# Kernel tuning notes

Hardware: AMD Instinct MI355X
Metric: run time of the kernel (lower is better)

Reference implementation:

```python
import jax, jax.numpy as jnp
import numpy as np

B, S, D, H = 2, 2048, 1024, 16
D_H = D // H  # 64


def setup_inputs() -> dict:
    key = jax.random.key(0)
    ks = jax.random.split(key, 12)
    inp = {
        "query": jax.random.normal(ks[0], (B, S, D), dtype=jnp.float32),
        "key":   jax.random.normal(ks[1], (B, S, D), dtype=jnp.float32),
        "value": jax.random.normal(ks[2], (B, S, D), dtype=jnp.float32),
        # causal 0/1 float mask, broadcastable to [B, H, Sq, Sk]; 1 = masked
        "mask":  jnp.broadcast_to(jnp.triu(jnp.ones((S, S), dtype=jnp.float32), k=1)[None, None], (B, 1, S, S)),
    }
    scale = 0.02
    inp["wq"] = jax.random.normal(ks[3], (D, D), dtype=jnp.float32) * scale
    inp["bq"] = jnp.zeros((D,), dtype=jnp.float32)
    inp["wk"] = jax.random.normal(ks[4], (D, D), dtype=jnp.float32) * scale
    inp["bk"] = jnp.zeros((D,), dtype=jnp.float32)
    inp["wv"] = jax.random.normal(ks[5], (D, D), dtype=jnp.float32) * scale
    inp["bv"] = jnp.zeros((D,), dtype=jnp.float32)
    inp["wff"] = jax.random.normal(ks[6], (D, D), dtype=jnp.float32) * scale
    inp["bff"] = jnp.zeros((D,), dtype=jnp.float32)
    return inp


def _split_head(x):
    # [B, S, D] -> [B, H, S, d_h]
    b, s, _ = x.shape
    return x.reshape(b, s, H, D_H).transpose(0, 2, 1, 3)


def reference(query, key, value, mask, wq, bq, wk, bk, wv, bv, wff, bff):
    # QKV projections (torch Linear: x @ W.T + b)
    q = _split_head(query @ wq.T + bq)
    k = _split_head(key @ wk.T + bk)
    v = _split_head(value @ wv.T + bv)
    # scaled dot-product attention
    scores = jnp.einsum("bhqd,bhkd->bhqk", q, k) / jnp.sqrt(jnp.float32(D_H))
    scores = scores + mask * (-1e9)
    attn = jax.nn.softmax(scores, axis=-1)
    out = jnp.einsum("bhqk,bhkd->bhqd", attn, v)
    # concat heads: [B, H, S, d_h] -> [B, S, D]
    out = out.transpose(0, 2, 1, 3).reshape(query.shape[0], query.shape[1], D)
    return out @ wff.T + bff
```

## Files before the change

kernel.cpp:

```cpp
#include <hip/hip_runtime.h>
#include <hip/hip_bf16.h>

#define B_  2
#define S_  2048
#define D_  1024
#define H_  16
#define DH_ 64
#define M_  (B_ * S_)

using bf16x8 = __attribute__((ext_vector_type(8))) short;
using s16x4  = __attribute__((ext_vector_type(4))) short;
using f32x4  = __attribute__((ext_vector_type(4))) float;

__device__ __forceinline__ bf16x8 ldg8(const __hip_bfloat16* p) {
    bf16x8 v;
    __builtin_memcpy(&v, p, 16);
    return v;
}
__device__ __forceinline__ bf16x8 lds8(const __hip_bfloat16* p) {
    bf16x8 v;
    __builtin_memcpy(&v, p, 16);
    return v;
}
__device__ __forceinline__ void gll16(const void* g, void* l) {
    __builtin_amdgcn_global_load_lds(
        (const __attribute__((address_space(1))) unsigned int*)g,
        (__attribute__((address_space(3))) unsigned int*)l,
        16, 0, 0);
}
__device__ __forceinline__ short bf16bits(float x) {
    __hip_bfloat16 hv = __float2bfloat16(x);
    short sv;
    __builtin_memcpy(&sv, &hv, 2);
    return sv;
}
__device__ __forceinline__ unsigned cvtpk(float lo, float hi) {
    unsigned r;
    asm("v_cvt_pk_bf16_f32 %0, %1, %2" : "=v"(r) : "v"(lo), "v"(hi));
    return r;
}

__global__ void cvt_all(const float* __restrict__ q, const float* __restrict__ k,
                        const float* __restrict__ v, const float* __restrict__ wq,
                        const float* __restrict__ wk, const float* __restrict__ wv,
                        const float* __restrict__ wff,
                        __hip_bfloat16* __restrict__ Xq, __hip_bfloat16* __restrict__ Xk,
                        __hip_bfloat16* __restrict__ Xv, __hip_bfloat16* __restrict__ Wq,
                        __hip_bfloat16* __restrict__ Wk, __hip_bfloat16* __restrict__ Wv,
                        __hip_bfloat16* __restrict__ Wf) {
    const size_t e = (size_t)(blockIdx.x * 256 + threadIdx.x) * 8;
    const float* src;
    __hip_bfloat16* dst;
    size_t off;
    if (e < ((size_t)3 << 22)) {
        const int i = (int)(e >> 22);
        off = e & (((size_t)1 << 22) - 1);
        src = (i == 0) ? q : (i == 1) ? k : v;
        dst = (i == 0) ? Xq : (i == 1) ? Xk : Xv;
    } else {
        const size_t e2 = e - ((size_t)3 << 22);
        const int i = (int)(e2 >> 20);
        off = e2 & (((size_t)1 << 20) - 1);
        src = (i == 0) ? wq : (i == 1) ? wk : (i == 2) ? wv : wff;
        dst = (i == 0) ? Wq : (i == 1) ? Wk : (i == 2) ? Wv : Wf;
    }
    float4 a, b;
    __builtin_memcpy(&a, src + off, 16);
    __builtin_memcpy(&b, src + off + 4, 16);
    __hip_bfloat16 h[8];
    h[0] = __float2bfloat16(a.x); h[1] = __float2bfloat16(a.y);
    h[2] = __float2bfloat16(a.z); h[3] = __float2bfloat16(a.w);
    h[4] = __float2bfloat16(b.x); h[5] = __float2bfloat16(b.y);
    h[6] = __float2bfloat16(b.z); h[7] = __float2bfloat16(b.w);
    __builtin_memcpy(dst + off, h, 16);
}

template<int MI>
__device__ __forceinline__
void gemm_body(const __hip_bfloat16* __restrict__ A,
               const __hip_bfloat16* __restrict__ W,
               const float* __restrict__ bias,
               void* __restrict__ out, int mode, float oscale,
               int row0, int col0) {
    constexpr int K  = D_;
    constexpr int N  = D_;
    constexpr int TM = MI * 32;
    __shared__ __hip_bfloat16 At[2][TM][32];
    __shared__ __hip_bfloat16 Wt[2][128][32];

    const int tid = threadIdx.x;
    const int w   = tid >> 6;
    const int l   = tid & 63;
    const int lr  = l & 15;
    const int lg  = l >> 4;
    const int wr  = (w >> 1) * (MI * 16);
    const int wc  = (w & 1) * 64;

    const int srow   = l >> 2;
    const int schunk = l & 3;

    f32x4 acc[MI][4] = {};

    auto STAGE = [&](int buf, int k0) {
#pragma unroll
        for (int r = 0; r < TM / 64; ++r) {
            const int row = r * 64 + w * 16 + srow;
            const int csw = (schunk ^ (row & 3)) * 8;
            gll16(A + (size_t)(row0 + row) * K + k0 + csw, &At[buf][r * 64 + w * 16][0]);
        }
#pragma unroll
        for (int r = 0; r < 2; ++r) {
            const int row = r * 64 + w * 16 + srow;
            const int csw = (schunk ^ (row & 3)) * 8;
            gll16(W + (size_t)(col0 + row) * K + k0 + csw, &Wt[buf][r * 64 + w * 16][0]);
        }
    };

    STAGE(0, 0);
    int cur = 0;
    for (int k0 = 0; k0 < K; k0 += 32) {
        __syncthreads();
        if (k0 + 32 < K) STAGE(cur ^ 1, k0 + 32);
        bf16x8 af[MI], wf[4];
#pragma unroll
        for (int m = 0; m < MI; ++m) {
            const int arow = wr + m * 16 + lr;
            af[m] = lds8(&At[cur][arow][(lg ^ (arow & 3)) * 8]);
        }
#pragma unroll
        for (int n = 0; n < 4; ++n) {
            const int wrow = wc + n * 16 + lr;
            wf[n] = lds8(&Wt[cur][wrow][(lg ^ (wrow & 3)) * 8]);
        }
#pragma unroll
        for (int m = 0; m < MI; ++m)
#pragma unroll
            for (int n = 0; n < 4; ++n)
                acc[m][n] = __builtin_amdgcn_mfma_f32_16x16x32_bf16(
                    af[m], wf[n], acc[m][n], 0, 0, 0);
        cur ^= 1;
    }

    float bv[4];
#pragma unroll
    for (int n = 0; n < 4; ++n) bv[n] = bias[col0 + wc + n * 16 + lr];

    if (mode == 1) {
#pragma unroll
        for (int m = 0; m < MI; ++m) {
            const int row_s = row0 + wr + m * 16 + lg * 4;
            const int bq = row_s >> 11, s0 = row_s & (S_ - 1);
#pragma unroll
            for (int n = 0; n < 4; ++n) {
                const int col = col0 + wc + n * 16 + lr;
                const int h = col >> 6, d = col & (DH_ - 1);
                s16x4 pk;
#pragma unroll
                for (int r = 0; r < 4; ++r) pk[r] = bf16bits(acc[m][n][r] + bv[n]);
                __builtin_memcpy(
                    (__hip_bfloat16*)out + ((size_t)((bq * H_ + h) * DH_) + d) * S_ + s0,
                    &pk, 8);
            }
        }
    } else {
#pragma unroll
        for (int m = 0; m < MI; ++m)
#pragma unroll
            for (int n = 0; n < 4; ++n)
#pragma unroll
                for (int r = 0; r < 4; ++r) {
                    const int row = row0 + wr + m * 16 + lg * 4 + r;
                    const int col = col0 + wc + n * 16 + lr;
                    const float v = acc[m][n][r] + bv[n];
                    if (mode == 0)
                        ((__hip_bfloat16*)out)[(size_t)row * N + col] =
                            __float2bfloat16(v * oscale);
                    else
                        ((float*)out)[(size_t)row * N + col] = v;
                }
    }
}

__global__ __launch_bounds__(256)
void gemm_qkv(const __hip_bfloat16* __restrict__ Xq, const __hip_bfloat16* __restrict__ Xk,
              const __hip_bfloat16* __restrict__ Xv, const __hip_bfloat16* __restrict__ Wq,
              const __hip_bfloat16* __restrict__ Wk, const __hip_bfloat16* __restrict__ Wv,
              const float* __restrict__ bq, const float* __restrict__ bk,
              const float* __restrict__ bv,
              __hip_bfloat16* __restrict__ Qp, __hip_bfloat16* __restrict__ Kp,
              __hip_bfloat16* __restrict__ Vt) {
    const int z = blockIdx.z;
    const __hip_bfloat16* A = (z == 0) ? Xq : (z == 1) ? Xk : Xv;
    const __hip_bfloat16* W = (z == 0) ? Wq : (z == 1) ? Wk : Wv;
    const float* bias       = (z == 0) ? bq : (z == 1) ? bk : bv;
    void* out               = (z == 0) ? (void*)Qp : (z == 1) ? (void*)Kp : (void*)Vt;
    const float osc = (z == 0) ? 0.125f * 1.4426950408889634f : 1.f;

    const int lin  = blockIdx.y * 8 + blockIdx.x;
    const int xcd  = lin & 7;
    const int idx  = lin >> 3;
    const int row0 = (xcd * 4 + (idx & 3)) * 128;
    const int col0 = (idx >> 2) * 128;

    gemm_body<4>(A, W, bias, out, (z == 2) ? 1 : 0, osc, row0, col0);
}

__global__ __launch_bounds__(256)
void gemm_ff(const __hip_bfloat16* __restrict__ A, const __hip_bfloat16* __restrict__ W,
             const float* __restrict__ bias, float* __restrict__ out) {
    const int lin  = blockIdx.y * 8 + blockIdx.x;
    const int xcd  = lin & 7;
    const int idx  = lin >> 3;
    const int row0 = (xcd * 8 + (idx & 7)) * 64;
    const int col0 = (idx >> 3) * 128;
    gemm_body<2>(A, W, bias, out, 2, 1.f, row0, col0);
}

__global__ __launch_bounds__(512)
void attn_fwd(const __hip_bfloat16* __restrict__ Qp,
              const __hip_bfloat16* __restrict__ Kp,
              const __hip_bfloat16* __restrict__ Vt,
              __hip_bfloat16* __restrict__ O) {
    __shared__ __hip_bfloat16 Kt[2][64][64];
    __shared__ __hip_bfloat16 Vs[2][64][64];
    __shared__ __hip_bfloat16 Pl[8][16][64];

    const int tid = threadIdx.x;
    const int w   = tid >> 6;
    const int l   = tid & 63;
    const int lr  = l & 15;
    const int lg  = l >> 4;

    const int raw = blockIdx.x;
    const int wg  = (raw & 7) * 64 + (raw >> 3);
    const int xcd = wg >> 6;
    const int loc = wg & 63;
    const int bhi = loc >> 4;
    const int prr = loc & 15;
    const int pr  = (bhi >= 2) ? (15 - prr) : prr;
    const int bh  = xcd * 4 + bhi;
    const int h   = bh & (H_ - 1);
    const int b   = bh >> 4;

    const int sub  = w >> 2;
    const int qb_s = sub ? (31 - pr) : pr;
    const int qw0  = qb_s * 64 + (w & 3) * 16;

    bf16x8 aq[2];
#pragma unroll
    for (int kc = 0; kc < 2; ++kc)
        aq[kc] = ldg8(Qp + (size_t)(b * S_ + qw0 + lr) * D_ + h * DH_ + kc * 32 + lg * 8);

    f32x4 o[4] = {};
    f32x4 rs4 = {};

    const int nkt_max = 32 - pr;

    const int srow   = l >> 3;
    const int schunk = l & 7;
    const int psw    = (lr & 7) << 4;

    auto STAGE = [&](int buf, int kt) {
        const int k0 = kt * 64;
        const int row = w * 8 + srow;
        const int csw = (schunk ^ (row & 7)) * 8;
        gll16(Kp + (size_t)(b * S_ + k0 + row) * D_ + h * DH_ + csw,
              &Kt[buf][w * 8][0]);
        gll16(Vt + ((size_t)((b * H_ + h) * DH_) + row) * S_ + k0 + csw,
              &Vs[buf][w * 8][0]);
    };

    char* prow = (char*)&Pl[w][lr][0];

    auto STEP = [&](int kt, int cur) {
        const int k0 = kt * 64;
        __syncthreads();
        if (kt + 1 < nkt_max) STAGE(cur ^ 1, kt + 1);

        if (kt <= qb_s) {
            f32x4 sc[4] = {};
            __builtin_amdgcn_s_setprio(1);
#pragma unroll
            for (int kk = 0; kk < 4; ++kk) {
                const int krow = kk * 16 + lr;
#pragma unroll
                for (int kc = 0; kc < 2; ++kc) {
                    bf16x8 kf = lds8(&Kt[cur][krow][((kc * 4 + lg) ^ (krow & 7)) * 8]);
                    sc[kk] = __builtin_amdgcn_mfma_f32_16x16x32_bf16(kf, aq[kc], sc[kk], 0, 0, 0);
                }
            }
            __builtin_amdgcn_s_setprio(0);

            const int qrow = qw0 + lr;
            if (kt == qb_s) {
#pragma unroll
                for (int kk = 0; kk < 4; ++kk) {
                    float pv[4];
#pragma unroll
                    for (int r = 0; r < 4; ++r) {
                        const int key = k0 + kk * 16 + lg * 4 + r;
                        pv[r] = (key > qrow) ? 0.f : exp2f(sc[kk][r]);
                        rs4[r] += pv[r];
                    }
                    unsigned uu[2] = { cvtpk(pv[0], pv[1]), cvtpk(pv[2], pv[3]) };
                    __builtin_memcpy(prow + ((kk * 32 + lg * 8) ^ psw), uu, 8);
                }
            } else {
#pragma unroll
                for (int kk = 0; kk < 4; ++kk) {
                    float pv[4];
#pragma unroll
                    for (int r = 0; r < 4; ++r) {
                        pv[r] = exp2f(sc[kk][r]);
                        rs4[r] += pv[r];
                    }
                    unsigned uu[2] = { cvtpk(pv[0], pv[1]), cvtpk(pv[2], pv[3]) };
                    __builtin_memcpy(prow + ((kk * 32 + lg * 8) ^ psw), uu, 8);
                }
            }

            bf16x8 pa[2];
#pragma unroll
            for (int kc = 0; kc < 2; ++kc)
                __builtin_memcpy(&pa[kc], prow + ((kc * 64 + lg * 16) ^ psw), 16);
            __builtin_amdgcn_s_setprio(1);
#pragma unroll
            for (int j = 0; j < 4; ++j) {
                const int vrow = j * 16 + lr;
#pragma unroll
                for (int kc = 0; kc < 2; ++kc) {
                    bf16x8 vf = lds8(&Vs[cur][vrow][((kc * 4 + lg) ^ (vrow & 7)) * 8]);
                    o[j] = __builtin_amdgcn_mfma_f32_16x16x32_bf16(pa[kc], vf, o[j], 0, 0, 0);
                }
            }
            __builtin_amdgcn_s_setprio(0);
        }
    };

    STAGE(0, 0);
    for (int kt = 0; kt < nkt_max; kt += 2) {
        STEP(kt, 0);
        if (kt + 1 < nkt_max) STEP(kt + 1, 1);
    }

    float rsf = rs4[0] + rs4[1] + rs4[2] + rs4[3];
    rsf += __shfl_xor(rsf, 16);
    rsf += __shfl_xor(rsf, 32);
#pragma unroll
    for (int r = 0; r < 4; ++r) {
        const float inv = 1.f / __shfl(rsf, 4 * lg + r);
        const int row = qw0 + 4 * lg + r;
#pragma unroll
        for (int j = 0; j < 4; ++j)
            O[((size_t)(b * S_ + row)) * D_ + h * DH_ + j * 16 + lr] =
                __float2bfloat16(o[j][r] * inv);
    }
}

extern "C" void kernel_launch(void* const* d_in, const int* in_sizes, int n_in,
                              void* d_out, int out_size, void* d_ws, size_t ws_size,
                              hipStream_t stream) {
    const float* q    = (const float*)d_in[0];
    const float* kin  = (const float*)d_in[1];
    const float* vin  = (const float*)d_in[2];
    const float* wq   = (const float*)d_in[4];
    const float* bq   = (const float*)d_in[5];
    const float* wk   = (const float*)d_in[6];
    const float* bk   = (const float*)d_in[7];
    const float* wv   = (const float*)d_in[8];
    const float* bv   = (const float*)d_in[9];
    const float* wff  = (const float*)d_in[10];
    const float* bff  = (const float*)d_in[11];

    char* ws = (char*)d_ws;
    const size_t MB = 1024 * 1024;
    __hip_bfloat16* Xq  = (__hip_bfloat16*)(ws + 0 * MB);
    __hip_bfloat16* Xk  = (__hip_bfloat16*)(ws + 8 * MB);
    __hip_bfloat16* Xv  = (__hip_bfloat16*)(ws + 16 * MB);
    __hip_bfloat16* Wqb = (__hip_bfloat16*)(ws + 24 * MB);
    __hip_bfloat16* Wkb = (__hip_bfloat16*)(ws + 26 * MB);
    __hip_bfloat16* Wvb = (__hip_bfloat16*)(ws + 28 * MB);
    __hip_bfloat16* Wfb = (__hip_bfloat16*)(ws + 30 * MB);
    __hip_bfloat16* Qp  = (__hip_bfloat16*)(ws + 32 * MB);
    __hip_bfloat16* Kp  = (__hip_bfloat16*)(ws + 40 * MB);
    __hip_bfloat16* Vt  = (__hip_bfloat16*)(ws + 48 * MB);
    __hip_bfloat16* Ob  = (__hip_bfloat16*)(ws + 56 * MB);

    cvt_all<<<8192, 256, 0, stream>>>(q, kin, vin, wq, wk, wv, wff,
                                      Xq, Xk, Xv, Wqb, Wkb, Wvb, Wfb);

    dim3 gq(8, 32, 3);
    gemm_qkv<<<gq, 256, 0, stream>>>(Xq, Xk, Xv, Wqb, Wkb, Wvb,
                                     bq, bk, bv, Qp, Kp, Vt);

    attn_fwd<<<512, 512, 0, stream>>>(Qp, Kp, Vt, Ob);

    dim3 gg(8, 64);
    gemm_ff<<<gg, 256, 0, stream>>>(Ob, Wfb, bff, (float*)d_out);
}
```

Baseline: 119.6 us.

## Balance causal attention work by splitting high query block keys across wave groups

Each workgroup still owns a paired low and high query block, but the work is now split differently. The first four waves process the low block and then the first part of the high block's key range. The second four waves process the remaining key tiles of the high block, and each group has its own double-buffered K/V stream. At the end the partial outputs and row sums are combined through shared memory, which replaces the earlier pattern where half the waves sat idle on masked tiles. In exchange the kernel uses twice the LDS for K/V, adds a cross-group reduction, and relies on softmax without a running max, since the partial sums are added directly.

```diff
diff --git a/kernel.cpp b/kernel.cpp
--- a/kernel.cpp
+++ b/kernel.cpp
@@ -221,8 +221,8 @@
               const __hip_bfloat16* __restrict__ Kp,
               const __hip_bfloat16* __restrict__ Vt,
               __hip_bfloat16* __restrict__ O) {
-    __shared__ __hip_bfloat16 Kt[2][64][64];
-    __shared__ __hip_bfloat16 Vs[2][64][64];
+    __shared__ __hip_bfloat16 Kt[2][2][64][64];
+    __shared__ __hip_bfloat16 Vs[2][2][64][64];
     __shared__ __hip_bfloat16 Pl[8][16][64];
 
     const int tid = threadIdx.x;
@@ -230,130 +230,182 @@
     const int l   = tid & 63;
     const int lr  = l & 15;
     const int lg  = l >> 4;
+    const int grp = w >> 2;
+    const int wi  = w & 3;
 
     const int raw = blockIdx.x;
     const int wg  = (raw & 7) * 64 + (raw >> 3);
-    const int xcd = wg >> 6;
-    const int loc = wg & 63;
-    const int bhi = loc >> 4;
-    const int prr = loc & 15;
-    const int pr  = (bhi >= 2) ? (15 - prr) : prr;
-    const int bh  = xcd * 4 + bhi;
+    const int bh  = wg >> 4;
+    const int pr  = wg & 15;
     const int h   = bh & (H_ - 1);
     const int b   = bh >> 4;
 
-    const int sub  = w >> 2;
-    const int qb_s = sub ? (31 - pr) : pr;
-    const int qw0  = qb_s * 64 + (w & 3) * 16;
-
-    bf16x8 aq[2];
-#pragma unroll
-    for (int kc = 0; kc < 2; ++kc)
-        aq[kc] = ldg8(Qp + (size_t)(b * S_ + qw0 + lr) * D_ + h * DH_ + kc * 32 + lg * 8);
-
-    f32x4 o[4] = {};
-    f32x4 rs4 = {};
-
-    const int nkt_max = 32 - pr;
+    const int qbL = pr, qbH = 31 - pr;
+    const int qwL = qbL * 64 + wi * 16;
+    const int qwH = qbH * 64 + wi * 16;
 
     const int srow   = l >> 3;
     const int schunk = l & 7;
     const int psw    = (lr & 7) << 4;
 
-    auto STAGE = [&](int buf, int kt) {
+    bf16x8 aqH[2], aqL[2];
+#pragma unroll
+    for (int kc = 0; kc < 2; ++kc)
+        aqH[kc] = ldg8(Qp + (size_t)(b * S_ + qwH + lr) * D_ + h * DH_ + kc * 32 + lg * 8);
+    if (grp == 0) {
+#pragma unroll
+        for (int kc = 0; kc < 2; ++kc)
+            aqL[kc] = ldg8(Qp + (size_t)(b * S_ + qwL + lr) * D_ + h * DH_ + kc * 32 + lg * 8);
+    }
+
+    f32x4 oH[4] = {}, oL[4] = {};
+    f32x4 rsH4 = {}, rsL4 = {};
+
+    auto STAGE = [&](int stream, int buf, int kt) {
         const int k0 = kt * 64;
-        const int row = w * 8 + srow;
-        const int csw = (schunk ^ (row & 7)) * 8;
-        gll16(Kp + (size_t)(b * S_ + k0 + row) * D_ + h * DH_ + csw,
-              &Kt[buf][w * 8][0]);
-        gll16(Vt + ((size_t)((b * H_ + h) * DH_) + row) * S_ + k0 + csw,
-              &Vs[buf][w * 8][0]);
+#pragma unroll
+        for (int r = 0; r < 2; ++r) {
+            const int row = wi * 16 + r * 8 + srow;
+            const int csw = (schunk ^ (row & 7)) * 8;
+            gll16(Kp + (size_t)(b * S_ + k0 + row) * D_ + h * DH_ + csw,
+                  &Kt[stream][buf][wi * 16 + r * 8][0]);
+            gll16(Vt + ((size_t)((b * H_ + h) * DH_) + row) * S_ + k0 + csw,
+                  &Vs[stream][buf][wi * 16 + r * 8][0]);
+        }
     };
 
     char* prow = (char*)&Pl[w][lr][0];
 
-    auto STEP = [&](int kt, int cur) {
+    auto UNIT = [&](int stream, int curb, int kt, const bf16x8 (&aq)[2],
+                    f32x4 (&o)[4], f32x4& rs4, int qw0, bool diag) {
         const int k0 = kt * 64;
+        f32x4 sc[4] = {};
+        __builtin_amdgcn_s_setprio(1);
+#pragma unroll
+        for (int kk = 0; kk < 4; ++kk) {
+            const int krow = kk * 16 + lr;
+#pragma unroll
+            for (int kc = 0; kc < 2; ++kc) {
+                bf16x8 kf = lds8(&Kt[stream][curb][krow][((kc * 4 + lg) ^ (krow & 7)) * 8]);
+                sc[kk] = __builtin_amdgcn_mfma_f32_16x16x32_bf16(kf, aq[kc], sc[kk], 0, 0, 0);
+            }
+        }
+        __builtin_amdgcn_s_setprio(0);
+
+        const int qrow = qw0 + lr;
+        if (diag) {
+#pragma unroll
+            for (int kk = 0; kk < 4; ++kk) {
+                float pv[4];
+#pragma unroll
+                for (int r = 0; r < 4; ++r) {
+                    const int key = k0 + kk * 16 + lg * 4 + r;
+                    pv[r] = (key > qrow) ? 0.f : exp2f(sc[kk][r]);
+                    rs4[r] += pv[r];
+                }
+                unsigned uu[2] = { cvtpk(pv[0], pv[1]), cvtpk(pv[2], pv[3]) };
+                __builtin_memcpy(prow + ((kk * 32 + lg * 8) ^ psw), uu, 8);
+            }
+        } else {
+#pragma unroll
+            for (int kk = 0; kk < 4; ++kk) {
+                float pv[4];
+#pragma unroll
+                for (int r = 0; r < 4; ++r) {
+                    pv[r] = exp2f(sc[kk][r]);
+                    rs4[r] += pv[r];
+                }
+                unsigned uu[2] = { cvtpk(pv[0], pv[1]), cvtpk(pv[2], pv[3]) };
+                __builtin_memcpy(prow + ((kk * 32 + lg * 8) ^ psw), uu, 8);
+            }
+        }
+
+        bf16x8 pa[2];
+#pragma unroll
+        for (int kc = 0; kc < 2; ++kc)
+            __builtin_memcpy(&pa[kc], prow + ((kc * 64 + lg * 16) ^ psw), 16);
+        __builtin_amdgcn_s_setprio(1);
+#pragma unroll
+        for (int j = 0; j < 4; ++j) {
+            const int vrow = j * 16 + lr;
+#pragma unroll
+            for (int kc = 0; kc < 2; ++kc) {
+                bf16x8 vf = lds8(&Vs[stream][curb][vrow][((kc * 4 + lg) ^ (vrow & 7)) * 8]);
+                o[j] = __builtin_amdgcn_mfma_f32_16x16x32_bf16(pa[kc], vf, o[j], 0, 0, 0);
+            }
+        }
+        __builtin_amdgcn_s_setprio(0);
+    };
+
+    auto STEP = [&](int s, int curb) {
         __syncthreads();
-        if (kt + 1 < nkt_max) STAGE(cur ^ 1, kt + 1);
-
-        if (kt <= qb_s) {
-            f32x4 sc[4] = {};
-            __builtin_amdgcn_s_setprio(1);
-#pragma unroll
-            for (int kk = 0; kk < 4; ++kk) {
-                const int krow = kk * 16 + lr;
-#pragma unroll
-                for (int kc = 0; kc < 2; ++kc) {
-                    bf16x8 kf = lds8(&Kt[cur][krow][((kc * 4 + lg) ^ (krow & 7)) * 8]);
-                    sc[kk] = __builtin_amdgcn_mfma_f32_16x16x32_bf16(kf, aq[kc], sc[kk], 0, 0, 0);
-                }
-            }
-            __builtin_amdgcn_s_setprio(0);
-
-            const int qrow = qw0 + lr;
-            if (kt == qb_s) {
-#pragma unroll
-                for (int kk = 0; kk < 4; ++kk) {
-                    float pv[4];
-#pragma unroll
-                    for (int r = 0; r < 4; ++r) {
-                        const int key = k0 + kk * 16 + lg * 4 + r;
-                        pv[r] = (key > qrow) ? 0.f : exp2f(sc[kk][r]);
-                        rs4[r] += pv[r];
-                    }
-                    unsigned uu[2] = { cvtpk(pv[0], pv[1]), cvtpk(pv[2], pv[3]) };
-                    __builtin_memcpy(prow + ((kk * 32 + lg * 8) ^ psw), uu, 8);
-                }
-            } else {
-#pragma unroll
-                for (int kk = 0; kk < 4; ++kk) {
-                    float pv[4];
-#pragma unroll
-                    for (int r = 0; r < 4; ++r) {
-                        pv[r] = exp2f(sc[kk][r]);
-                        rs4[r] += pv[r];
-                    }
-                    unsigned uu[2] = { cvtpk(pv[0], pv[1]), cvtpk(pv[2], pv[3]) };
-                    __builtin_memcpy(prow + ((kk * 32 + lg * 8) ^ psw), uu, 8);
-                }
-            }
-
-            bf16x8 pa[2];
-#pragma unroll
-            for (int kc = 0; kc < 2; ++kc)
-                __builtin_memcpy(&pa[kc], prow + ((kc * 64 + lg * 16) ^ psw), 16);
-            __builtin_amdgcn_s_setprio(1);
-#pragma unroll
-            for (int j = 0; j < 4; ++j) {
-                const int vrow = j * 16 + lr;
-#pragma unroll
-                for (int kc = 0; kc < 2; ++kc) {
-                    bf16x8 vf = lds8(&Vs[cur][vrow][((kc * 4 + lg) ^ (vrow & 7)) * 8]);
-                    o[j] = __builtin_amdgcn_mfma_f32_16x16x32_bf16(pa[kc], vf, o[j], 0, 0, 0);
-                }
-            }
-            __builtin_amdgcn_s_setprio(0);
+        if (grp == 0) {
+            if (s + 1 < 17) {
+                const int nkt = (s + 1 <= pr) ? (s + 1) : (s - pr);
+                STAGE(0, curb ^ 1, nkt);
+            }
+            if (s <= pr) UNIT(0, curb, s, aqL, oL, rsL4, qwL, s == pr);
+            else         UNIT(0, curb, s - pr - 1, aqH, oH, rsH4, qwH, false);
+        } else {
+            if (s + 1 < 16) STAGE(1, curb ^ 1, 16 - pr + s + 1);
+            if (s < 16)     UNIT(1, curb, 16 - pr + s, aqH, oH, rsH4, qwH, s == 15);
         }
     };
 
-    STAGE(0, 0);
-    for (int kt = 0; kt < nkt_max; kt += 2) {
-        STEP(kt, 0);
-        if (kt + 1 < nkt_max) STEP(kt + 1, 1);
-    }
-
-    float rsf = rs4[0] + rs4[1] + rs4[2] + rs4[3];
-    rsf += __shfl_xor(rsf, 16);
-    rsf += __shfl_xor(rsf, 32);
-#pragma unroll
-    for (int r = 0; r < 4; ++r) {
-        const float inv = 1.f / __shfl(rsf, 4 * lg + r);
-        const int row = qw0 + 4 * lg + r;
+    if (grp == 0) STAGE(0, 0, 0);
+    else          STAGE(1, 0, 16 - pr);
+
+    for (int s = 0; s < 17; s += 2) {
+        STEP(s, 0);
+        if (s + 1 < 17) STEP(s + 1, 1);
+    }
+
+    auto rsum = [&](const f32x4& v) {
+        float x = v[0] + v[1] + v[2] + v[3];
+        x += __shfl_xor(x, 16);
+        x += __shfl_xor(x, 32);
+        return x;
+    };
+
+    float* Ox = (float*)&Kt[1][0][0][0];
+    float* Rx = (float*)&Vs[1][0][0][0];
+
+    if (grp == 1) {
+        const float rsf = rsum(rsH4);
 #pragma unroll
         for (int j = 0; j < 4; ++j)
-            O[((size_t)(b * S_ + row)) * D_ + h * DH_ + j * 16 + lr] =
-                __float2bfloat16(o[j][r] * inv);
+#pragma unroll
+            for (int r = 0; r < 4; ++r)
+                Ox[(wi * 16 + 4 * lg + r) * 64 + j * 16 + lr] = oH[j][r];
+        if (l < 16) Rx[wi * 16 + lr] = rsf;
+    }
+    __syncthreads();
+    if (grp == 0) {
+        const float rsfL = rsum(rsL4);
+#pragma unroll
+        for (int r = 0; r < 4; ++r) {
+            const float inv = 1.f / __shfl(rsfL, 4 * lg + r);
+            const int row = qwL + 4 * lg + r;
+#pragma unroll
+            for (int j = 0; j < 4; ++j)
+                O[((size_t)(b * S_ + row)) * D_ + h * DH_ + j * 16 + lr] =
+                    __float2bfloat16(oL[j][r] * inv);
+        }
+        const float tot = rsum(rsH4) + Rx[wi * 16 + lr];
+#pragma unroll
+        for (int j = 0; j < 4; ++j)
+#pragma unroll
+            for (int r = 0; r < 4; ++r)
+                oH[j][r] += Ox[(wi * 16 + 4 * lg + r) * 64 + j * 16 + lr];
+#pragma unroll
+        for (int r = 0; r < 4; ++r) {
+            const float inv = 1.f / __shfl(tot, 4 * lg + r);
+            const int row = qwH + 4 * lg + r;
+#pragma unroll
+            for (int j = 0; j < 4; ++j)
+                O[((size_t)(b * S_ + row)) * D_ + h * DH_ + j * 16 + lr] =
+                    __float2bfloat16(oH[j][r] * inv);
+        }
     }
 }
 
```

Measured after the change: 119.3 us. No clear change (-0.2%).

## Fuse fp32-to-bf16 activation conversion into QKV GEMM tile loads

Applied to the files above, without the earlier changes.

The separate pass that converted the query/key/value activations to bf16 is removed. The QKV GEMM now stages fp32 activation tiles straight into LDS with an 8-chunk XOR swizzle and packs them to bf16 with v_cvt_pk_bf16_f32 just before the MFMA. This drops a full read and write of the activations plus the re-read of the bf16 copies. In exchange the GEMM loads twice the bytes per A tile, uses twice the LDS for it, and does extra conversion work in the inner loop.

```diff
diff --git a/kernel.cpp b/kernel.cpp
--- a/kernel.cpp
+++ b/kernel.cpp
@@ -17,8 +17,13 @@
     __builtin_memcpy(&v, p, 16);
     return v;
 }
-__device__ __forceinline__ bf16x8 lds8(const __hip_bfloat16* p) {
+__device__ __forceinline__ bf16x8 lds8(const void* p) {
     bf16x8 v;
+    __builtin_memcpy(&v, p, 16);
+    return v;
+}
+__device__ __forceinline__ f32x4 lds4f(const void* p) {
+    f32x4 v;
     __builtin_memcpy(&v, p, 16);
     return v;
 }
@@ -40,30 +45,15 @@
     return r;
 }
 
-__global__ void cvt_all(const float* __restrict__ q, const float* __restrict__ k,
-                        const float* __restrict__ v, const float* __restrict__ wq,
-                        const float* __restrict__ wk, const float* __restrict__ wv,
-                        const float* __restrict__ wff,
-                        __hip_bfloat16* __restrict__ Xq, __hip_bfloat16* __restrict__ Xk,
-                        __hip_bfloat16* __restrict__ Xv, __hip_bfloat16* __restrict__ Wq,
-                        __hip_bfloat16* __restrict__ Wk, __hip_bfloat16* __restrict__ Wv,
-                        __hip_bfloat16* __restrict__ Wf) {
+__global__ void cvt_w(const float* __restrict__ wq, const float* __restrict__ wk,
+                      const float* __restrict__ wv, const float* __restrict__ wff,
+                      __hip_bfloat16* __restrict__ Wq, __hip_bfloat16* __restrict__ Wk,
+                      __hip_bfloat16* __restrict__ Wv, __hip_bfloat16* __restrict__ Wf) {
     const size_t e = (size_t)(blockIdx.x * 256 + threadIdx.x) * 8;
-    const float* src;
-    __hip_bfloat16* dst;
-    size_t off;
-    if (e < ((size_t)3 << 22)) {
-        const int i = (int)(e >> 22);
-        off = e & (((size_t)1 << 22) - 1);
-        src = (i == 0) ? q : (i == 1) ? k : v;
-        dst = (i == 0) ? Xq : (i == 1) ? Xk : Xv;
-    } else {
-        const size_t e2 = e - ((size_t)3 << 22);
-        const int i = (int)(e2 >> 20);
-        off = e2 & (((size_t)1 << 20) - 1);
-        src = (i == 0) ? wq : (i == 1) ? wk : (i == 2) ? wv : wff;
-        dst = (i == 0) ? Wq : (i == 1) ? Wk : (i == 2) ? Wv : Wf;
-    }
+    const int i = (int)(e >> 20);
+    const size_t off = e & (((size_t)1 << 20) - 1);
+    const float* src = (i == 0) ? wq : (i == 1) ? wk : (i == 2) ? wv : wff;
+    __hip_bfloat16* dst = (i == 0) ? Wq : (i == 1) ? Wk : (i == 2) ? Wv : Wf;
     float4 a, b;
     __builtin_memcpy(&a, src + off, 16);
     __builtin_memcpy(&b, src + off + 4, 16);
@@ -75,9 +65,9 @@
     __builtin_memcpy(dst + off, h, 16);
 }
 
-template<int MI>
+template<int MI, bool AF32>
 __device__ __forceinline__
-void gemm_body(const __hip_bfloat16* __restrict__ A,
+void gemm_body(const void* __restrict__ Ap,
                const __hip_bfloat16* __restrict__ W,
                const float* __restrict__ bias,
                void* __restrict__ out, int mode, float oscale,
@@ -85,7 +75,8 @@
     constexpr int K  = D_;
     constexpr int N  = D_;
     constexpr int TM = MI * 32;
-    __shared__ __hip_bfloat16 At[2][TM][32];
+    constexpr int AB = AF32 ? 128 : 64;
+    __shared__ __align__(16) char At[2][TM][AB];
     __shared__ __hip_bfloat16 Wt[2][128][32];
 
     const int tid = threadIdx.x;
@@ -96,22 +87,35 @@
     const int wr  = (w >> 1) * (MI * 16);
     const int wc  = (w & 1) * 64;
 
-    const int srow   = l >> 2;
-    const int schunk = l & 3;
+    const int srow4  = l >> 2;
+    const int schk4  = l & 3;
+    const int srow8  = l >> 3;
+    const int schk8  = l & 7;
 
     f32x4 acc[MI][4] = {};
 
     auto STAGE = [&](int buf, int k0) {
-#pragma unroll
-        for (int r = 0; r < TM / 64; ++r) {
-            const int row = r * 64 + w * 16 + srow;
-            const int csw = (schunk ^ (row & 3)) * 8;
-            gll16(A + (size_t)(row0 + row) * K + k0 + csw, &At[buf][r * 64 + w * 16][0]);
+        if (AF32) {
+#pragma unroll
+            for (int r = 0; r < TM / 32; ++r) {
+                const int row = r * 32 + w * 8 + srow8;
+                const int csw = (schk8 ^ (row & 7)) * 4;
+                gll16((const float*)Ap + (size_t)(row0 + row) * K + k0 + csw,
+                      &At[buf][r * 32 + w * 8][0]);
+            }
+        } else {
+#pragma unroll
+            for (int r = 0; r < TM / 64; ++r) {
+                const int row = r * 64 + w * 16 + srow4;
+                const int csw = (schk4 ^ (row & 3)) * 8;
+                gll16((const __hip_bfloat16*)Ap + (size_t)(row0 + row) * K + k0 + csw,
+                      &At[buf][r * 64 + w * 16][0]);
+            }
         }
 #pragma unroll
         for (int r = 0; r < 2; ++r) {
-            const int row = r * 64 + w * 16 + srow;
-            const int csw = (schunk ^ (row & 3)) * 8;
+            const int row = r * 64 + w * 16 + srow4;
+            const int csw = (schk4 ^ (row & 3)) * 8;
             gll16(W + (size_t)(col0 + row) * K + k0 + csw, &Wt[buf][r * 64 + w * 16][0]);
         }
     };
@@ -125,7 +129,17 @@
 #pragma unroll
         for (int m = 0; m < MI; ++m) {
             const int arow = wr + m * 16 + lr;
-            af[m] = lds8(&At[cur][arow][(lg ^ (arow & 3)) * 8]);
+            if (AF32) {
+                const int c0 = (2 * lg) ^ (arow & 7);
+                const int c1 = (2 * lg + 1) ^ (arow & 7);
+                f32x4 a0 = lds4f(&At[cur][arow][c0 * 16]);
+                f32x4 a1 = lds4f(&At[cur][arow][c1 * 16]);
+                unsigned uu[4] = { cvtpk(a0[0], a0[1]), cvtpk(a0[2], a0[3]),
+                                   cvtpk(a1[0], a1[1]), cvtpk(a1[2], a1[3]) };
+                __builtin_memcpy(&af[m], uu, 16);
+            } else {
+                af[m] = lds8(&At[cur][arow][((lg ^ (arow & 3)) * 8) * 2]);
+            }
         }
 #pragma unroll
         for (int n = 0; n < 4; ++n) {
@@ -182,15 +196,15 @@
 }
 
 __global__ __launch_bounds__(256)
-void gemm_qkv(const __hip_bfloat16* __restrict__ Xq, const __hip_bfloat16* __restrict__ Xk,
-              const __hip_bfloat16* __restrict__ Xv, const __hip_bfloat16* __restrict__ Wq,
+void gemm_qkv(const float* __restrict__ Xq, const float* __restrict__ Xk,
+              const float* __restrict__ Xv, const __hip_bfloat16* __restrict__ Wq,
               const __hip_bfloat16* __restrict__ Wk, const __hip_bfloat16* __restrict__ Wv,
               const float* __restrict__ bq, const float* __restrict__ bk,
               const float* __restrict__ bv,
               __hip_bfloat16* __restrict__ Qp, __hip_bfloat16* __restrict__ Kp,
               __hip_bfloat16* __restrict__ Vt) {
     const int z = blockIdx.z;
-    const __hip_bfloat16* A = (z == 0) ? Xq : (z == 1) ? Xk : Xv;
+    const void* A           = (z == 0) ? (const void*)Xq : (z == 1) ? (const void*)Xk : (const void*)Xv;
     const __hip_bfloat16* W = (z == 0) ? Wq : (z == 1) ? Wk : Wv;
     const float* bias       = (z == 0) ? bq : (z == 1) ? bk : bv;
     void* out               = (z == 0) ? (void*)Qp : (z == 1) ? (void*)Kp : (void*)Vt;
@@ -202,7 +216,7 @@
     const int row0 = (xcd * 4 + (idx & 3)) * 128;
     const int col0 = (idx >> 2) * 128;
 
-    gemm_body<4>(A, W, bias, out, (z == 2) ? 1 : 0, osc, row0, col0);
+    gemm_body<4, true>(A, W, bias, out, (z == 2) ? 1 : 0, osc, row0, col0);
 }
 
 __global__ __launch_bounds__(256)
@@ -213,7 +227,7 @@
     const int idx  = lin >> 3;
     const int row0 = (xcd * 8 + (idx & 7)) * 64;
     const int col0 = (idx >> 3) * 128;
-    gemm_body<2>(A, W, bias, out, 2, 1.f, row0, col0);
+    gemm_body<2, false>(A, W, bias, out, 2, 1.f, row0, col0);
 }
 
 __global__ __launch_bounds__(512)
@@ -374,9 +388,6 @@
 
     char* ws = (char*)d_ws;
     const size_t MB = 1024 * 1024;
-    __hip_bfloat16* Xq  = (__hip_bfloat16*)(ws + 0 * MB);
-    __hip_bfloat16* Xk  = (__hip_bfloat16*)(ws + 8 * MB);
-    __hip_bfloat16* Xv  = (__hip_bfloat16*)(ws + 16 * MB);
     __hip_bfloat16* Wqb = (__hip_bfloat16*)(ws + 24 * MB);
     __hip_bfloat16* Wkb = (__hip_bfloat16*)(ws + 26 * MB);
     __hip_bfloat16* Wvb = (__hip_bfloat16*)(ws + 28 * MB);
@@ -386,11 +397,10 @@
     __hip_bfloat16* Vt  = (__hip_bfloat16*)(ws + 48 * MB);
     __hip_bfloat16* Ob  = (__hip_bfloat16*)(ws + 56 * MB);
 
-    cvt_all<<<8192, 256, 0, stream>>>(q, kin, vin, wq, wk, wv, wff,
-                                      Xq, Xk, Xv, Wqb, Wkb, Wvb, Wfb);
+    cvt_w<<<2048, 256, 0, stream>>>(wq, wk, wv, wff, Wqb, Wkb, Wvb, Wfb);
 
     dim3 gq(8, 32, 3);
-    gemm_qkv<<<gq, 256, 0, stream>>>(Xq, Xk, Xv, Wqb, Wkb, Wvb,
+    gemm_qkv<<<gq, 256, 0, stream>>>(q, kin, vin, Wqb, Wkb, Wvb,
                                      bq, bk, bv, Qp, Kp, Vt);
 
     attn_fwd<<<512, 512, 0, stream>>>(Qp, Kp, Vt, Ob);
```

Result: faster. 114.5 us (median of 2 runs) (-4.3%).
